# Kernel optimization log

Hardware: AMD Instinct MI355X
Metric: run time of the kernel (lower is better)

Reference implementation:

```python
import jax, jax.numpy as jnp
import numpy as np

B, T, S, H, V, L = 32, 64, 128, 512, 32000, 2  # batch, tgt_len, src_len, d_model, vocab, n_layers


def setup_inputs() -> dict:
    key = jax.random.key(0)
    ks = jax.random.split(key, 14)
    sc = 1.0 / np.sqrt(H)
    tgt = jax.random.randint(ks[0], (B, T), 0, V, dtype=jnp.int32)
    h0 = jax.random.normal(ks[1], (L, B, H), jnp.float32)
    c0 = jax.random.normal(ks[2], (L, B, H), jnp.float32)
    encoder_outputs = jax.random.normal(ks[3], (B, S, H), jnp.float32)
    emb = (jax.random.normal(ks[4], (V, H), jnp.float32) * 0.02).at[0].set(0.0)  # pad_idx=0 row zeroed
    W_ih = jax.random.normal(ks[5], (L, 4 * H, H), jnp.float32) * sc  # gate order i,f,g,o (torch)
    W_hh = jax.random.normal(ks[6], (L, 4 * H, H), jnp.float32) * sc
    b_ih = jax.random.normal(ks[7], (L, 4 * H), jnp.float32) * sc
    b_hh = jax.random.normal(ks[8], (L, 4 * H), jnp.float32) * sc
    Wc = jax.random.normal(ks[9], (H, 2 * H), jnp.float32) * sc
    bc = jax.random.normal(ks[10], (H,), jnp.float32) * sc
    Wo = jax.random.normal(ks[11], (V, H), jnp.float32) * sc
    bo = jax.random.normal(ks[12], (V,), jnp.float32) * sc
    return dict(tgt=tgt, h0=h0, c0=c0, encoder_outputs=encoder_outputs, emb=emb,
                W_ih=W_ih, W_hh=W_hh, b_ih=b_ih, b_hh=b_hh, Wc=Wc, bc=bc, Wo=Wo, bo=bo)


def reference(tgt, h0, c0, encoder_outputs, emb, W_ih, W_hh, b_ih, b_hh, Wc, bc, Wo, bo):
    n_layers = W_ih.shape[0]

    def step(carry, token):
        h, c = carry  # each [L, B, H]
        x = emb[token]  # [B, H]
        hs, cs = [], []
        for l in range(n_layers):  # small fixed structural loop
            gates = x @ W_ih[l].T + b_ih[l] + h[l] @ W_hh[l].T + b_hh[l]  # [B, 4H]
            i_g, f_g, g_g, o_g = jnp.split(gates, 4, axis=-1)
            c_new = jax.nn.sigmoid(f_g) * c[l] + jax.nn.sigmoid(i_g) * jnp.tanh(g_g)
            h_new = jax.nn.sigmoid(o_g) * jnp.tanh(c_new)
            hs.append(h_new)
            cs.append(c_new)
            x = h_new
        out = x  # [B, H] top-layer output
        # Luong (dot) attention over encoder outputs
        scores = jnp.einsum('bh,bsh->bs', out, encoder_outputs)
        attn = jax.nn.softmax(scores, axis=-1)
        context = jnp.einsum('bs,bsh->bh', attn, encoder_outputs)
        out_att = jnp.tanh(jnp.concatenate([out, context], axis=-1) @ Wc.T + bc)
        pred = out_att @ Wo.T + bo  # [B, V]
        return (jnp.stack(hs), jnp.stack(cs)), pred

    (h, c), preds = jax.lax.scan(step, (h0, c0), tgt.T)  # scan over time (T-major)
    return preds.transpose(1, 0, 2), h, c  # [B, T, V], hidden state
```

## Files before the change

kernel.cpp:

```cpp
#include <hip/hip_runtime.h>
#include <hip/hip_bf16.h>

#define Bz 32
#define Tz 64
#define Sz 128
#define Hz 512
#define Vz 32000
#define G4 2048
#define NBLK 256
#define NPH 65

#define A_RLX __ATOMIC_RELAXED
#define SC_AG __HIP_MEMORY_SCOPE_AGENT

using bf16x8 = __attribute__((ext_vector_type(8))) short;
using f32x4  = __attribute__((ext_vector_type(4))) float;

__device__ __forceinline__ unsigned short f2bf(float f){
  unsigned int u = __float_as_uint(f);
  u += 0x7fffu + ((u >> 16) & 1u);
  return (unsigned short)(u >> 16);
}
__device__ __forceinline__ float sigf(float x){ return 1.f/(1.f + expf(-x)); }

__device__ __forceinline__ void stc(float* p, float v){
  __hip_atomic_store(p, v, A_RLX, SC_AG);
}
__device__ __forceinline__ float ldc(const float* p){
  return __hip_atomic_load(p, A_RLX, SC_AG);
}

__device__ __forceinline__ void gbar(unsigned* bar, int bid, unsigned* ep){
  asm volatile("s_waitcnt vmcnt(0)" ::: "memory");
  __syncthreads();
  const unsigned e = ++(*ep);
  const int tid = threadIdx.x;
  if (bid == 0){
    if (tid >= 1 && tid < 256){
      while (__hip_atomic_load(&bar[tid*4], A_RLX, SC_AG) != e)
        __builtin_amdgcn_s_sleep(1);
    }
    __syncthreads();
    if (tid < 256)
      __hip_atomic_store(&bar[1024 + tid*16], e, A_RLX, SC_AG);
  } else {
    if (tid == 0){
      __hip_atomic_store(&bar[bid*4], e, A_RLX, SC_AG);
      while (__hip_atomic_load(&bar[1024 + bid*16], A_RLX, SC_AG) != e)
        __builtin_amdgcn_s_sleep(1);
    }
  }
  __syncthreads();
  __builtin_amdgcn_sched_barrier(0);
}

__device__ __forceinline__ void xreduce(float (&a)[32], int lane){
  #pragma unroll
  for (int j = 0; j < 32; j++) a[j] += __shfl_xor(a[j], 32);
  #pragma unroll
  for (int st = 0; st < 5; st++){
    const int o = 16 >> st;
    bool hi = (lane & o) != 0;
    float tmp[16];
    #pragma unroll
    for (int j = 0; j < o; j++){
      float lo_v = a[j], hi_v = a[j + o];
      float sent = hi ? lo_v : hi_v;
      float recv = __shfl_xor(sent, o);
      tmp[j] = (hi ? hi_v : lo_v) + recv;
    }
    #pragma unroll
    for (int j = 0; j < o; j++) a[j] = tmp[j];
  }
}

__device__ __forceinline__ void stage2c(float* dA, const float* sA,
                                        float* dB, const float* sB, int tid){
  float ra[32], rb[32];
  #pragma unroll
  for (int i = 0; i < 32; i++) ra[i] = ldc(sA + tid + i*512);
  #pragma unroll
  for (int i = 0; i < 32; i++) rb[i] = ldc(sB + tid + i*512);
  #pragma unroll
  for (int i = 0; i < 32; i++){
    int f = tid + i*512;
    dA[(f >> 9)*520 + (f & 511)] = ra[i];
  }
  #pragma unroll
  for (int i = 0; i < 32; i++){
    int f = tid + i*512;
    dB[(f >> 9)*520 + (f & 511)] = rb[i];
  }
}

__global__ __launch_bounds__(256) void init_state_v8(const float* __restrict__ h0,
    float* __restrict__ h0p, float* __restrict__ h1p, unsigned int* __restrict__ bar){
  int i = blockIdx.x*256 + threadIdx.x;
  if (i < 16384) h0p[16384 + i] = h0[i];
  else           h1p[3*16384 + (i - 16384)] = h0[i];
  if (i < 5120) bar[i] = 0u;
}

__global__ __launch_bounds__(256) void conv_bf16_kernel(const float* __restrict__ src,
    unsigned short* __restrict__ dst){
  int i = (blockIdx.x*256 + threadIdx.x)*4;
  float4 v = *(const float4*)(src + i);
  ushort4 o;
  o.x = f2bf(v.x); o.y = f2bf(v.y); o.z = f2bf(v.z); o.w = f2bf(v.w);
  *(ushort4*)(dst + i) = o;
}

__global__ __launch_bounds__(256) void pack_l0_v3(const float* __restrict__ W,
    float* __restrict__ out){
  int idx4 = blockIdx.x*256 + threadIdx.x;
  int r = idx4 >> 7, k4 = idx4 & 127;
  int srow = (r & 3)*Hz + (r >> 2);
  ((float4*)out)[idx4] = ((const float4*)W)[srow*128 + k4];
}
__global__ __launch_bounds__(256) void pack_l1_v3(const float* __restrict__ Wi,
    const float* __restrict__ Wh, float* __restrict__ out){
  int idx4 = blockIdx.x*256 + threadIdx.x;
  int r = idx4 >> 8, k4 = idx4 & 255;
  int srow = (r & 3)*Hz + (r >> 2);
  float4 v = (k4 < 128) ? ((const float4*)Wi)[srow*128 + k4]
                        : ((const float4*)Wh)[srow*128 + (k4 - 128)];
  ((float4*)out)[idx4] = v;
}

__global__ __launch_bounds__(256) void x0g_v3(const int* __restrict__ tgt,
    const float* __restrict__ emb, const float* __restrict__ W,
    const float* __restrict__ bi, const float* __restrict__ bh,
    float* __restrict__ out){
  __shared__ float As[32][68], Bs[32][68];
  __shared__ int tok_s[64];
  int tid = threadIdx.x;
  int m0 = blockIdx.y*64, n0 = blockIdx.x*64;
  if (tid < 64){ int tb = m0 + tid; tok_s[tid] = tgt[(tb & 31)*Tz + (tb >> 5)]; }
  __syncthreads();
  int lm = tid >> 2, lk = (tid & 3)*8;
  int ty = tid >> 4, tx = tid & 15;
  float acc[4][4] = {{0.f}};
  for (int kt = 0; kt < 16; kt++){
    float4 a0 = *(const float4*)(emb + (size_t)tok_s[lm]*Hz + kt*32 + lk);
    float4 a1 = *(const float4*)(emb + (size_t)tok_s[lm]*Hz + kt*32 + lk + 4);
    float4 b0 = *(const float4*)(W   + (size_t)(n0+lm)*Hz + kt*32 + lk);
    float4 b1 = *(const float4*)(W   + (size_t)(n0+lm)*Hz + kt*32 + lk + 4);
    __syncthreads();
    As[lk+0][lm]=a0.x; As[lk+1][lm]=a0.y; As[lk+2][lm]=a0.z; As[lk+3][lm]=a0.w;
    As[lk+4][lm]=a1.x; As[lk+5][lm]=a1.y; As[lk+6][lm]=a1.z; As[lk+7][lm]=a1.w;
    Bs[lk+0][lm]=b0.x; Bs[lk+1][lm]=b0.y; Bs[lk+2][lm]=b0.z; Bs[lk+3][lm]=b0.w;
    Bs[lk+4][lm]=b1.x; Bs[lk+5][lm]=b1.y; Bs[lk+6][lm]=b1.z; Bs[lk+7][lm]=b1.w;
    __syncthreads();
    #pragma unroll
    for (int k = 0; k < 32; k++){
      float4 av = *(const float4*)&As[k][ty*4];
      float4 bv = *(const float4*)&Bs[k][tx*4];
      acc[0][0]+=av.x*bv.x; acc[0][1]+=av.x*bv.y; acc[0][2]+=av.x*bv.z; acc[0][3]+=av.x*bv.w;
      acc[1][0]+=av.y*bv.x; acc[1][1]+=av.y*bv.y; acc[1][2]+=av.y*bv.z; acc[1][3]+=av.y*bv.w;
      acc[2][0]+=av.z*bv.x; acc[2][1]+=av.z*bv.y; acc[2][2]+=av.z*bv.z; acc[2][3]+=av.z*bv.w;
      acc[3][0]+=av.w*bv.x; acc[3][1]+=av.w*bv.y; acc[3][2]+=av.w*bv.z; acc[3][3]+=av.w*bv.w;
    }
  }
  #pragma unroll
  for (int j = 0; j < 4; j++){
    int col = n0 + tx*4 + j;
    float bias = bi[col] + bh[col];
    #pragma unroll
    for (int i = 0; i < 4; i++){
      int tb = m0 + ty*4 + i;
      int tt = tb >> 5, bb = tb & 31;
      out[((size_t)tt*2048 + col)*32 + bb] = acc[i][j] + bias;
    }
  }
}

__global__ __launch_bounds__(512, 1) void decoder_persist_v8(
    const float* __restrict__ Wp0, const float* __restrict__ Wp1,
    const float* x0gT,
    const float* __restrict__ bi1, const float* __restrict__ bh1,
    const float* __restrict__ c0in,
    float* __restrict__ h0p,
    float* __restrict__ h1p,
    float* hist,
    float* __restrict__ cbuf,
    unsigned* __restrict__ bar){
  extern __shared__ float sm[];
  float* hstA = sm;
  float* hstB = sm + 16640;
  float* gsA  = sm + 33280;
  float* gsB  = sm + 33792;
  float4* hA4 = (float4*)hstA;
  float4* hB4 = (float4*)hstB;

  const int bid = blockIdx.x, tid = threadIdx.x;
  const int w4 = tid >> 6, lane = tid & 63;
  const int kh = w4 >> 2, rpair = w4 & 3;
  const int r0 = bid*8 + rpair*2, r1 = r0 + 1;
  unsigned ep = 0;

  const float4* Wp0_4 = (const float4*)Wp0;
  const float4* Wp1_4 = (const float4*)Wp1;
  float4 w0A  = Wp0_4[r0*128 + kh*64 + lane];
  float4 w0B  = Wp0_4[r1*128 + kh*64 + lane];
  float4 w1xA = Wp1_4[r0*256 +       kh*64 + lane];
  float4 w1xB = Wp1_4[r1*256 +       kh*64 + lane];
  float4 w1hA = Wp1_4[r0*256 + 128 + kh*64 + lane];
  float4 w1hB = Wp1_4[r1*256 + 128 + kh*64 + lane];
  float bs_i=0.f, bs_f=0.f, bs_g=0.f, bs_o=0.f;
  float c0_reg=0.f, c1_reg=0.f;
  if (tid < 64){
    int b = tid & 31, u = bid*2 + (tid >> 5);
    bs_i = bi1[u]        + bh1[u];
    bs_f = bi1[512+u]    + bh1[512+u];
    bs_g = bi1[1024+u]   + bh1[1024+u];
    bs_o = bi1[1536+u]   + bh1[1536+u];
    c0_reg = c0in[b*512 + u];
    c1_reg = c0in[16384 + b*512 + u];
  }
  __syncthreads();

  for (int tau = 0; tau < NPH; ++tau){
    stage2c(hstA, h0p + ((tau+1)&1)*16384, hstB, h1p + ((tau+2)&3)*16384, tid);
    float xgi=0.f, xgf=0.f, xgg=0.f, xgo=0.f;
    if (tau < 64 && tid < 64){
      int b = tid & 31, u = bid*2 + (tid >> 5);
      const float* xg = x0gT + (size_t)tau*65536;
      xgi = xg[(u       )*32 + b];
      xgf = xg[(512  + u)*32 + b];
      xgg = xg[(1024 + u)*32 + b];
      xgo = xg[(1536 + u)*32 + b];
    }
    __syncthreads();
    {
      float aL0A[32], aL0B[32], aL1A[32], aL1B[32];
      #pragma unroll
      for (int b = 0; b < 32; b++){ aL0A[b]=0.f; aL0B[b]=0.f; aL1A[b]=0.f; aL1B[b]=0.f; }
      const float4* pA = hA4 + kh*64 + lane;
      const float4* pB = hB4 + kh*64 + lane;
      #pragma unroll
      for (int b = 0; b < 32; b++){
        float4 ha = pA[b*130];
        float4 hb = pB[b*130];
        aL0A[b] = fmaf(ha.x,w0A.x, fmaf(ha.y,w0A.y, fmaf(ha.z,w0A.z, fmaf(ha.w,w0A.w, aL0A[b]))));
        aL0B[b] = fmaf(ha.x,w0B.x, fmaf(ha.y,w0B.y, fmaf(ha.z,w0B.z, fmaf(ha.w,w0B.w, aL0B[b]))));
        float t1 = fmaf(ha.x,w1xA.x, fmaf(ha.y,w1xA.y, fmaf(ha.z,w1xA.z, fmaf(ha.w,w1xA.w, aL1A[b]))));
        aL1A[b] = fmaf(hb.x,w1hA.x, fmaf(hb.y,w1hA.y, fmaf(hb.z,w1hA.z, fmaf(hb.w,w1hA.w, t1))));
        float t2 = fmaf(ha.x,w1xB.x, fmaf(ha.y,w1xB.y, fmaf(ha.z,w1xB.z, fmaf(ha.w,w1xB.w, aL1B[b]))));
        aL1B[b] = fmaf(hb.x,w1hB.x, fmaf(hb.y,w1hB.y, fmaf(hb.z,w1hB.z, fmaf(hb.w,w1hB.w, t2))));
      }
      xreduce(aL0A, lane); xreduce(aL0B, lane);
      gsA[kh*256 + (rpair*2 + (lane >= 32 ? 1 : 0))*32 + (lane & 31)] = (lane < 32) ? aL0A[0] : aL0B[0];
      xreduce(aL1A, lane); xreduce(aL1B, lane);
      gsB[kh*256 + (rpair*2 + (lane >= 32 ? 1 : 0))*32 + (lane & 31)] = (lane < 32) ? aL1A[0] : aL1B[0];
    }
    __syncthreads();
    if (tid < 64){
      int ul = tid >> 5, b = tid & 31, u = bid*2 + ul, rl = ul*4;
      if (tau < 64){
        float gi = gsA[(rl+0)*32+b] + gsA[256+(rl+0)*32+b] + xgi;
        float gf = gsA[(rl+1)*32+b] + gsA[256+(rl+1)*32+b] + xgf;
        float gg = gsA[(rl+2)*32+b] + gsA[256+(rl+2)*32+b] + xgg;
        float go = gsA[(rl+3)*32+b] + gsA[256+(rl+3)*32+b] + xgo;
        float cn = sigf(gf)*c0_reg + sigf(gi)*tanhf(gg);
        c0_reg = cn;
        stc(h0p + (tau&1)*16384 + b*512 + u, sigf(go)*tanhf(cn));
      }
      if (tau >= 1){
        int t1s = tau - 1;
        float gi = gsB[(rl+0)*32+b] + gsB[256+(rl+0)*32+b] + bs_i;
        float gf = gsB[(rl+1)*32+b] + gsB[256+(rl+1)*32+b] + bs_f;
        float gg = gsB[(rl+2)*32+b] + gsB[256+(rl+2)*32+b] + bs_g;
        float go = gsB[(rl+3)*32+b] + gsB[256+(rl+3)*32+b] + bs_o;
        float cn = sigf(gf)*c1_reg + sigf(gi)*tanhf(gg);
        c1_reg = cn;
        float hv = sigf(go)*tanhf(cn);
        stc(h1p + (t1s&3)*16384 + b*512 + u, hv);
        hist[(size_t)t1s*65536 + b*512 + u] = hv;
      }
    }
    gbar(bar, bid, &ep);
  }
  if (tid < 64){
    int b = tid & 31, u = bid*2 + (tid >> 5);
    cbuf[b*512 + u] = c0_reg;
    cbuf[16384 + b*512 + u] = c1_reg;
  }
}

__global__ __launch_bounds__(256) void attn_batch(const float* hist,
    const float* __restrict__ enc, float* ctxout){
  __shared__ float h_s[Hz], e_s[Sz], red_s[2];
  const int bid = blockIdx.x;
  const int t = bid >> 5, b = bid & 31, tid = threadIdx.x;
  const float* h1 = hist + (size_t)t*65536 + b*512;
  *(float2*)(h_s + tid*2) = *(const float2*)(h1 + tid*2);
  __syncthreads();
  {
    int s = tid >> 1, half = tid & 1;
    const float4* e4 = (const float4*)(enc + ((size_t)b*Sz + s)*Hz + half*256);
    const float4* h4 = (const float4*)(h_s + half*256);
    float a = 0.f;
    #pragma unroll 16
    for (int k = 0; k < 64; k++){
      float4 e = e4[k], h = h4[k];
      a += e.x*h.x + e.y*h.y + e.z*h.z + e.w*h.w;
    }
    a += __shfl_xor(a, 1);
    if (!half) e_s[s] = a;
  }
  __syncthreads();
  if (tid < 64){
    float v = fmaxf(e_s[tid], e_s[tid+64]);
    #pragma unroll
    for (int o = 32; o; o >>= 1) v = fmaxf(v, __shfl_xor(v, o));
    if (tid == 0) red_s[0] = v;
  }
  __syncthreads();
  if (tid < Sz) e_s[tid] = expf(e_s[tid] - red_s[0]);
  __syncthreads();
  if (tid < 64){
    float v = e_s[tid] + e_s[tid+64];
    #pragma unroll
    for (int o = 32; o; o >>= 1) v += __shfl_xor(v, o);
    if (tid == 0) red_s[1] = v;
  }
  __syncthreads();
  {
    float inv = 1.f/red_s[1];
    int k0 = tid*2;
    float c0 = 0.f, c1 = 0.f;
    const float* ep = enc + (size_t)b*Sz*Hz + k0;
    #pragma unroll 8
    for (int s = 0; s < Sz; s++){
      float2 ev = *(const float2*)(ep + (size_t)s*Hz);
      float pr = e_s[s];
      c0 += pr*ev.x; c1 += pr*ev.y;
    }
    float2 o; o.x = c0*inv; o.y = c1*inv;
    *(float2*)(ctxout + (size_t)t*65536 + 32768 + b*512 + k0) = o;
  }
}

__global__ __launch_bounds__(256) void outatt_gemm(const float* xg,
    const float* __restrict__ Wc, const float* __restrict__ bc,
    unsigned short* __restrict__ oa){
  __shared__ float As[32][68], Bs[32][68];
  int tid = threadIdx.x;
  int m0 = blockIdx.y*64, n0 = blockIdx.x*64;
  int lm = tid >> 2, lk = (tid & 3)*8;
  int ty = tid >> 4, tx = tid & 15;
  int am = m0 + lm, at = am >> 5, ab = am & 31;
  const float* arow = xg + (size_t)at*65536 + ab*512;
  float acc[4][4] = {{0.f}};
  for (int kt = 0; kt < 32; kt++){
    int k = kt*32 + lk;
    const float* asrc = (k < 512) ? (arow + k) : (arow + 32768 + (k - 512));
    float4 a0 = *(const float4*)asrc;
    float4 a1 = *(const float4*)(asrc + 4);
    float4 b0 = *(const float4*)(Wc + (size_t)(n0+lm)*1024 + k);
    float4 b1 = *(const float4*)(Wc + (size_t)(n0+lm)*1024 + k + 4);
    __syncthreads();
    As[lk+0][lm]=a0.x; As[lk+1][lm]=a0.y; As[lk+2][lm]=a0.z; As[lk+3][lm]=a0.w;
    As[lk+4][lm]=a1.x; As[lk+5][lm]=a1.y; As[lk+6][lm]=a1.z; As[lk+7][lm]=a1.w;
    Bs[lk+0][lm]=b0.x; Bs[lk+1][lm]=b0.y; Bs[lk+2][lm]=b0.z; Bs[lk+3][lm]=b0.w;
    Bs[lk+4][lm]=b1.x; Bs[lk+5][lm]=b1.y; Bs[lk+6][lm]=b1.z; Bs[lk+7][lm]=b1.w;
    __syncthreads();
    #pragma unroll
    for (int k2 = 0; k2 < 32; k2++){
      float4 av = *(const float4*)&As[k2][ty*4];
      float4 bv = *(const float4*)&Bs[k2][tx*4];
      acc[0][0]+=av.x*bv.x; acc[0][1]+=av.x*bv.y; acc[0][2]+=av.x*bv.z; acc[0][3]+=av.x*bv.w;
      acc[1][0]+=av.y*bv.x; acc[1][1]+=av.y*bv.y; acc[1][2]+=av.y*bv.z; acc[1][3]+=av.y*bv.w;
      acc[2][0]+=av.z*bv.x; acc[2][1]+=av.z*bv.y; acc[2][2]+=av.z*bv.z; acc[2][3]+=av.z*bv.w;
      acc[3][0]+=av.w*bv.x; acc[3][1]+=av.w*bv.y; acc[3][2]+=av.w*bv.z; acc[3][3]+=av.w*bv.w;
    }
  }
  #pragma unroll
  for (int j = 0; j < 4; j++){
    int col = n0 + tx*4 + j;
    float bias = bc[col];
    #pragma unroll
    for (int i = 0; i < 4; i++){
      int m = m0 + ty*4 + i;
      int t = m >> 5, b = m & 31;
      oa[((size_t)(b*64 + t))*512 + col] = f2bf(tanhf(acc[i][j] + bias));
    }
  }
}

__global__ __launch_bounds__(256) void pred_gemm_v2(const unsigned short* __restrict__ A,
    const unsigned short* __restrict__ Bm, const float* __restrict__ bo,
    float* __restrict__ out){
  __shared__ unsigned short As[128*32];
  __shared__ unsigned short Bs[128*32];
  int bid = blockIdx.x;
  int xcd = bid & 7, lin = bid >> 3;
  int ntile = xcd*32 + (lin & 31);
  int mtile = lin >> 5;
  if (ntile >= 250) return;
  int n0 = ntile*128, m0 = mtile*128;
  int tid = threadIdx.x, lane = tid & 63, wid = tid >> 6;
  f32x4 acc[4][4];
  #pragma unroll
  for (int i = 0; i < 4; i++)
    #pragma unroll
    for (int j = 0; j < 4; j++)
      #pragma unroll
      for (int r = 0; r < 4; r++) acc[i][j][r] = 0.f;

  int wm = wid >> 1, wn = wid & 1;
  int r16 = lane & 15, kgr = lane >> 4;

  for (int kt = 0; kt < Hz/32; kt++){
    __syncthreads();
    #pragma unroll
    for (int call = 0; call < 2; call++){
      int c = call*256 + tid;
      int row = c >> 2, kg = c & 3;
      int kgs = kg ^ ((row >> 1) & 3);
      *(int4*)&As[row*32 + kgs*8] = *(const int4*)(A  + (size_t)(m0+row)*Hz + kt*32 + kg*8);
      *(int4*)&Bs[row*32 + kgs*8] = *(const int4*)(Bm + (size_t)(n0+row)*Hz + kt*32 + kg*8);
    }
    __syncthreads();
    bf16x8 aF[4], bF[4];
    #pragma unroll
    for (int i = 0; i < 4; i++){
      int ra = wm*64 + i*16 + r16;
      int rb = wn*64 + i*16 + r16;
      aF[i] = *(const bf16x8*)&As[ra*32 + (kgr ^ ((ra>>1)&3))*8];
      bF[i] = *(const bf16x8*)&Bs[rb*32 + (kgr ^ ((rb>>1)&3))*8];
    }
    #pragma unroll
    for (int i = 0; i < 4; i++)
      #pragma unroll
      for (int j = 0; j < 4; j++)
        acc[i][j] = __builtin_amdgcn_mfma_f32_16x16x32_bf16(aF[i], bF[j], acc[i][j], 0, 0, 0);
  }

  int rg = lane >> 4;
  #pragma unroll
  for (int i = 0; i < 4; i++)
    #pragma unroll
    for (int j = 0; j < 4; j++){
      int col = n0 + wn*64 + j*16 + r16;
      float bias = bo[col];
      #pragma unroll
      for (int r = 0; r < 4; r++){
        int row = m0 + wm*64 + i*16 + rg*4 + r;
        out[(size_t)row*Vz + col] = acc[i][j][r] + bias;
      }
    }
}

__global__ __launch_bounds__(256) void copy_hc_v4(const float* __restrict__ h0fin,
    const float* __restrict__ h1fin, const float* __restrict__ cbuf,
    float* __restrict__ out_hc){
  int i = blockIdx.x*256 + threadIdx.x;
  float v;
  if (i < 16384)      v = h0fin[i];
  else if (i < 32768) v = h1fin[i-16384];
  else                v = cbuf[i-32768];
  out_hc[i] = v;
}

extern "C" void kernel_launch(void* const* d_in, const int* in_sizes, int n_in,
                              void* d_out, int out_size, void* d_ws, size_t ws_size,
                              hipStream_t stream){
  const int*   tgt = (const int*)  d_in[0];
  const float* h0  = (const float*)d_in[1];
  const float* c0  = (const float*)d_in[2];
  const float* enc = (const float*)d_in[3];
  const float* emb = (const float*)d_in[4];
  const float* Wih = (const float*)d_in[5];
  const float* Whh = (const float*)d_in[6];
  const float* bih = (const float*)d_in[7];
  const float* bhh = (const float*)d_in[8];
  const float* Wc  = (const float*)d_in[9];
  const float* bc  = (const float*)d_in[10];
  const float* Wo  = (const float*)d_in[11];
  const float* bo  = (const float*)d_in[12];
  float* out = (float*)d_out;

  float* x0g  = (float*)d_ws;
  float* h0p  = x0g  + 4194304;
  float* h1p  = h0p  + 32768;
  float* cbuf = h1p  + 65536;
  float* Wp0  = cbuf + 32768;
  float* Wp1  = Wp0  + 1048576;
  unsigned int* bar = (unsigned int*)(Wp1 + 2097152);
  unsigned short* oa    = (unsigned short*)(bar + 5120);
  unsigned short* wo_bf = oa + 1048576;

  const int DLDS_BYTES = 34304 * 4;
  hipFuncSetAttribute((const void*)decoder_persist_v8,
      hipFuncAttributeMaxDynamicSharedMemorySize, DLDS_BYTES);

  init_state_v8<<<128, 256, 0, stream>>>(h0, h0p, h1p, bar);
  conv_bf16_kernel<<<16000, 256, 0, stream>>>(Wo, wo_bf);
  pack_l0_v3<<<1024, 256, 0, stream>>>(Whh, Wp0);
  pack_l1_v3<<<2048, 256, 0, stream>>>(Wih + (size_t)G4*Hz, Whh + (size_t)G4*Hz, Wp1);
  x0g_v3<<<dim3(32, 32), 256, 0, stream>>>(tgt, emb, Wih, bih, bhh, x0g);

  decoder_persist_v8<<<NBLK, 512, DLDS_BYTES, stream>>>(
      Wp0, Wp1, x0g, bih + G4, bhh + G4, c0,
      h0p, h1p, x0g, cbuf, (unsigned int*)bar);

  attn_batch<<<2048, 256, 0, stream>>>(x0g, enc, x0g);
  outatt_gemm<<<dim3(8, 32), 256, 0, stream>>>(x0g, Wc, bc, oa);
  pred_gemm_v2<<<4096, 256, 0, stream>>>(oa, wo_bf, bo, out);
  copy_hc_v4<<<256, 256, 0, stream>>>(h0p + 16384, x0g + (size_t)63*65536, cbuf,
                                      out + (size_t)Bz*Tz*Vz);

  (void)in_sizes; (void)n_in; (void)out_size; (void)ws_size;
}
```

Measured before the change: 1.115 ms.

## Split grid barrier into arrive/wait, overlap hist store and xg prefetch

Replaces the centralized two-hop grid barrier (block 0 gathers, then broadcasts) with a flat barrier. Each block publishes its epoch to its own slot, and one wavefront per block polls all 256 slots. Between arrive and wait, blocks store the history output and prefetch the next step's input-gate values, hiding that latency inside the barrier. It also reorders the pred GEMM tile mapping so consecutive blocks on an XCD share N tiles across M. The flat polling adds more atomic load traffic per block.

```diff
diff --git a/kernel.cpp b/kernel.cpp
--- a/kernel.cpp
+++ b/kernel.cpp
@@ -30,24 +30,24 @@
   return __hip_atomic_load(p, A_RLX, SC_AG);
 }
 
-__device__ __forceinline__ void gbar(unsigned* bar, int bid, unsigned* ep){
+__device__ __forceinline__ void g_arrive(unsigned* bar, int bid, unsigned e){
   asm volatile("s_waitcnt vmcnt(0)" ::: "memory");
   __syncthreads();
-  const unsigned e = ++(*ep);
-  const int tid = threadIdx.x;
-  if (bid == 0){
-    if (tid >= 1 && tid < 256){
-      while (__hip_atomic_load(&bar[tid*4], A_RLX, SC_AG) != e)
-        __builtin_amdgcn_s_sleep(1);
-    }
-    __syncthreads();
-    if (tid < 256)
-      __hip_atomic_store(&bar[1024 + tid*16], e, A_RLX, SC_AG);
-  } else {
-    if (tid == 0){
-      __hip_atomic_store(&bar[bid*4], e, A_RLX, SC_AG);
-      while (__hip_atomic_load(&bar[1024 + bid*16], A_RLX, SC_AG) != e)
-        __builtin_amdgcn_s_sleep(1);
+  if (threadIdx.x == 0)
+    __hip_atomic_store(&bar[bid], e, A_RLX, SC_AG);
+}
+__device__ __forceinline__ void g_wait(unsigned* bar, unsigned e){
+  if (threadIdx.x < 64){
+    const int lane = threadIdx.x;
+    for (;;){
+      int ok = 1;
+      #pragma unroll
+      for (int i = 0; i < 4; i++){
+        unsigned v = __hip_atomic_load(&bar[lane + i*64], A_RLX, SC_AG);
+        ok &= ((int)(v - e) >= 0);
+      }
+      if (__all(ok)) break;
+      __builtin_amdgcn_s_sleep(1);
     }
   }
   __syncthreads();
@@ -98,7 +98,7 @@
   int i = blockIdx.x*256 + threadIdx.x;
   if (i < 16384) h0p[16384 + i] = h0[i];
   else           h1p[3*16384 + (i - 16384)] = h0[i];
-  if (i < 5120) bar[i] = 0u;
+  if (i < 512) bar[i] = 0u;
 }
 
 __global__ __launch_bounds__(256) void conv_bf16_kernel(const float* __restrict__ src,
@@ -174,7 +174,7 @@
   }
 }
 
-__global__ __launch_bounds__(512, 1) void decoder_persist_v8(
+__global__ __launch_bounds__(512, 1) void decoder_persist_v9(
     const float* __restrict__ Wp0, const float* __restrict__ Wp1,
     const float* x0gT,
     const float* __restrict__ bi1, const float* __restrict__ bh1,
@@ -196,7 +196,6 @@
   const int w4 = tid >> 6, lane = tid & 63;
   const int kh = w4 >> 2, rpair = w4 & 3;
   const int r0 = bid*8 + rpair*2, r1 = r0 + 1;
-  unsigned ep = 0;
 
   const float4* Wp0_4 = (const float4*)Wp0;
   const float4* Wp1_4 = (const float4*)Wp1;
@@ -208,6 +207,7 @@
   float4 w1hB = Wp1_4[r1*256 + 128 + kh*64 + lane];
   float bs_i=0.f, bs_f=0.f, bs_g=0.f, bs_o=0.f;
   float c0_reg=0.f, c1_reg=0.f;
+  float xgi=0.f, xgf=0.f, xgg=0.f, xgo=0.f;
   if (tid < 64){
     int b = tid & 31, u = bid*2 + (tid >> 5);
     bs_i = bi1[u]        + bh1[u];
@@ -216,20 +216,15 @@
     bs_o = bi1[1536+u]   + bh1[1536+u];
     c0_reg = c0in[b*512 + u];
     c1_reg = c0in[16384 + b*512 + u];
+    xgi = x0gT[(u       )*32 + b];
+    xgf = x0gT[(512  + u)*32 + b];
+    xgg = x0gT[(1024 + u)*32 + b];
+    xgo = x0gT[(1536 + u)*32 + b];
   }
   __syncthreads();
 
   for (int tau = 0; tau < NPH; ++tau){
     stage2c(hstA, h0p + ((tau+1)&1)*16384, hstB, h1p + ((tau+2)&3)*16384, tid);
-    float xgi=0.f, xgf=0.f, xgg=0.f, xgo=0.f;
-    if (tau < 64 && tid < 64){
-      int b = tid & 31, u = bid*2 + (tid >> 5);
-      const float* xg = x0gT + (size_t)tau*65536;
-      xgi = xg[(u       )*32 + b];
-      xgf = xg[(512  + u)*32 + b];
-      xgg = xg[(1024 + u)*32 + b];
-      xgo = xg[(1536 + u)*32 + b];
-    }
     __syncthreads();
     {
       float aL0A[32], aL0B[32], aL1A[32], aL1B[32];
@@ -254,6 +249,7 @@
       gsB[kh*256 + (rpair*2 + (lane >= 32 ? 1 : 0))*32 + (lane & 31)] = (lane < 32) ? aL1A[0] : aL1B[0];
     }
     __syncthreads();
+    float hv1 = 0.f;
     if (tid < 64){
       int ul = tid >> 5, b = tid & 31, u = bid*2 + ul, rl = ul*4;
       if (tau < 64){
@@ -266,19 +262,30 @@
         stc(h0p + (tau&1)*16384 + b*512 + u, sigf(go)*tanhf(cn));
       }
       if (tau >= 1){
-        int t1s = tau - 1;
         float gi = gsB[(rl+0)*32+b] + gsB[256+(rl+0)*32+b] + bs_i;
         float gf = gsB[(rl+1)*32+b] + gsB[256+(rl+1)*32+b] + bs_f;
         float gg = gsB[(rl+2)*32+b] + gsB[256+(rl+2)*32+b] + bs_g;
         float go = gsB[(rl+3)*32+b] + gsB[256+(rl+3)*32+b] + bs_o;
         float cn = sigf(gf)*c1_reg + sigf(gi)*tanhf(gg);
         c1_reg = cn;
-        float hv = sigf(go)*tanhf(cn);
-        stc(h1p + (t1s&3)*16384 + b*512 + u, hv);
-        hist[(size_t)t1s*65536 + b*512 + u] = hv;
+        hv1 = sigf(go)*tanhf(cn);
+        stc(h1p + ((tau-1)&3)*16384 + b*512 + u, hv1);
       }
     }
-    gbar(bar, bid, &ep);
+    g_arrive(bar, bid, (unsigned)(tau + 1));
+    if (tid < 64){
+      int b = tid & 31, u = bid*2 + (tid >> 5);
+      if (tau >= 1)
+        hist[(size_t)(tau-1)*65536 + b*512 + u] = hv1;
+      if (tau + 1 < 64){
+        const float* xg = x0gT + (size_t)(tau+1)*65536;
+        xgi = xg[(u       )*32 + b];
+        xgf = xg[(512  + u)*32 + b];
+        xgg = xg[(1024 + u)*32 + b];
+        xgo = xg[(1536 + u)*32 + b];
+      }
+    }
+    g_wait(bar, (unsigned)(tau + 1));
   }
   if (tid < 64){
     int b = tid & 31, u = bid*2 + (tid >> 5);
@@ -388,15 +395,15 @@
   }
 }
 
-__global__ __launch_bounds__(256) void pred_gemm_v2(const unsigned short* __restrict__ A,
+__global__ __launch_bounds__(256) void pred_gemm_v3(const unsigned short* __restrict__ A,
     const unsigned short* __restrict__ Bm, const float* __restrict__ bo,
     float* __restrict__ out){
   __shared__ unsigned short As[128*32];
   __shared__ unsigned short Bs[128*32];
   int bid = blockIdx.x;
   int xcd = bid & 7, lin = bid >> 3;
-  int ntile = xcd*32 + (lin & 31);
-  int mtile = lin >> 5;
+  int ntile = xcd*32 + (lin >> 4);
+  int mtile = lin & 15;
   if (ntile >= 250) return;
   int n0 = ntile*128, m0 = mtile*128;
   int tid = threadIdx.x, lane = tid & 63, wid = tid >> 6;
@@ -488,11 +495,11 @@
   float* Wp0  = cbuf + 32768;
   float* Wp1  = Wp0  + 1048576;
   unsigned int* bar = (unsigned int*)(Wp1 + 2097152);
-  unsigned short* oa    = (unsigned short*)(bar + 5120);
+  unsigned short* oa    = (unsigned short*)(bar + 512);
   unsigned short* wo_bf = oa + 1048576;
 
   const int DLDS_BYTES = 34304 * 4;
-  hipFuncSetAttribute((const void*)decoder_persist_v8,
+  hipFuncSetAttribute((const void*)decoder_persist_v9,
       hipFuncAttributeMaxDynamicSharedMemorySize, DLDS_BYTES);
 
   init_state_v8<<<128, 256, 0, stream>>>(h0, h0p, h1p, bar);
@@ -501,13 +508,13 @@
   pack_l1_v3<<<2048, 256, 0, stream>>>(Wih + (size_t)G4*Hz, Whh + (size_t)G4*Hz, Wp1);
   x0g_v3<<<dim3(32, 32), 256, 0, stream>>>(tgt, emb, Wih, bih, bhh, x0g);
 
-  decoder_persist_v8<<<NBLK, 512, DLDS_BYTES, stream>>>(
+  decoder_persist_v9<<<NBLK, 512, DLDS_BYTES, stream>>>(
       Wp0, Wp1, x0g, bih + G4, bhh + G4, c0,
       h0p, h1p, x0g, cbuf, (unsigned int*)bar);
 
   attn_batch<<<2048, 256, 0, stream>>>(x0g, enc, x0g);
   outatt_gemm<<<dim3(8, 32), 256, 0, stream>>>(x0g, Wc, bc, oa);
-  pred_gemm_v2<<<4096, 256, 0, stream>>>(oa, wo_bf, bo, out);
+  pred_gemm_v3<<<4096, 256, 0, stream>>>(oa, wo_bf, bo, out);
   copy_hc_v4<<<256, 256, 0, stream>>>(h0p + 16384, x0g + (size_t)63*65536, cbuf,
                                       out + (size_t)Bz*Tz*Vz);
 
```

After: 1.285 ms. 15.3% more time.
